# Kernel optimization log

Measured on AMD Instinct MI355X. Metric: run time of the kernel, lower is better.

The kernel has to match this reference:

```python
import jax, jax.numpy as jnp
import numpy as np

C = 512        # num_channels
HEADS = 8      # num_channels // num_head_channels
DH = 64        # num_head_channels
G = 32         # num_groups
EPS = 1e-5
SCALE = DH ** -0.25  # pre-multiplied into q and k (scale applied twice -> 1/sqrt(DH))


def setup_inputs() -> dict:
    key = jax.random.key(0)
    ks = jax.random.split(key, 10)
    B, H, W = 2, 64, 64
    def w(k):
        return jax.random.normal(k, (C, C), jnp.float32) * 0.02
    def b(k):
        return jax.random.normal(k, (C,), jnp.float32) * 0.02
    return {
        "x": jax.random.normal(ks[0], (B, C, H, W), jnp.float32),
        "gn_w": jnp.ones((C,), jnp.float32),
        "gn_b": jnp.zeros((C,), jnp.float32),
        "wq": w(ks[1]), "bq": b(ks[2]),
        "wk": w(ks[3]), "bk": b(ks[4]),
        "wv": w(ks[5]), "bv": b(ks[6]),
        "wp": w(ks[7]), "bp": b(ks[8]),
    }


def reference(x, gn_w, gn_b, wq, bq, wk, bk, wv, bv, wp, bp):
    B, Cc, H, W = x.shape
    # GroupNorm over (C/G, H, W) per group
    xr = x.reshape(B, G, Cc // G, H * W)
    mean = xr.mean(axis=(2, 3), keepdims=True)
    var = xr.var(axis=(2, 3), keepdims=True)
    h = ((xr - mean) * jax.lax.rsqrt(var + EPS)).reshape(B, Cc, H, W)
    h = h * gn_w[None, :, None, None] + gn_b[None, :, None, None]
    # B C H W -> B (H W) C
    t = h.reshape(B, Cc, H * W).transpose(0, 2, 1)
    # q/k pre-multiplied by SCALE (equivalent to pre_multiply_weights_by_scale)
    q = (t @ wq.T + bq) * SCALE
    k = (t @ wk.T + bk) * SCALE
    v = t @ wv.T + bv
    def split_heads(a):  # B HW (h d) -> B h HW d
        return a.reshape(B, H * W, HEADS, DH).transpose(0, 2, 1, 3)
    q, k, v = split_heads(q), split_heads(k), split_heads(v)
    # full HWxHW score matrix, softmax over keys
    attn = jax.nn.softmax(jnp.einsum('bhqd,bhkd->bhqk', q, k), axis=-1)
    o = jnp.einsum('bhqk,bhkd->bhqd', attn, v)
    o = o.transpose(0, 2, 1, 3).reshape(B, H * W, Cc)  # join heads
    o = o @ wp.T + bp
    # B (H W) C -> B C H W, residual
    return o.transpose(0, 2, 1).reshape(B, Cc, H, W) + x
```

## Files before the change

kernel.cpp:

```cpp
#include <hip/hip_runtime.h>

#define HWN 4096
#define CCH 512
#define NHEAD 8
#define DHD 64
#define NBATCH 2
#define QK_SCALE 0.35355339059327373f
#define LOG2E    1.4426950408889634f

using floatx4 = __attribute__((ext_vector_type(4))) float;
using bf16x8  = __attribute__((ext_vector_type(8))) short;
using bf16x4  = __attribute__((ext_vector_type(4))) short;

__device__ __forceinline__ unsigned short f2b(float f) {
  union { float f; unsigned u; } x; x.f = f;
  unsigned r = x.u + 0x7FFFu + ((x.u >> 16) & 1u);
  return (unsigned short)(r >> 16);
}

__device__ __forceinline__ float fast_exp2(float x) {
#if __has_builtin(__builtin_amdgcn_exp2f)
  return __builtin_amdgcn_exp2f(x);
#else
  return __expf(x * 0.69314718056f);
#endif
}

__device__ __forceinline__ unsigned pack_bf16_trunc(float lo, float hi) {
  return __builtin_amdgcn_perm(__float_as_uint(hi), __float_as_uint(lo), 0x07060302u);
}

__global__ __launch_bounds__(256) void gn_stats(const float* __restrict__ x,
                                                float* __restrict__ stat) {
  int bg = blockIdx.x;
  const float4* p = (const float4*)(x + (size_t)bg * 65536) + blockIdx.y * 2048;
  float s = 0.f, ss = 0.f;
  for (int i = threadIdx.x; i < 2048; i += 256) {
    float4 v = p[i];
    s  += v.x + v.y + v.z + v.w;
    ss += v.x*v.x + v.y*v.y + v.z*v.z + v.w*v.w;
  }
  for (int off = 32; off; off >>= 1) {
    s  += __shfl_xor(s, off);
    ss += __shfl_xor(ss, off);
  }
  __shared__ float red[8];
  int w = threadIdx.x >> 6;
  if ((threadIdx.x & 63) == 0) { red[w] = s; red[4 + w] = ss; }
  __syncthreads();
  if (threadIdx.x == 0) {
    float S  = red[0] + red[1] + red[2] + red[3];
    float SS = red[4] + red[5] + red[6] + red[7];
    atomicAdd(&stat[bg], S);
    atomicAdd(&stat[64 + bg], SS);
  }
}

__global__ __launch_bounds__(256) void prep_w(
    const float* __restrict__ wq, const float* __restrict__ wk,
    const float* __restrict__ wv, const float* __restrict__ wp,
    const float* __restrict__ bq, const float* __restrict__ bk,
    const float* __restrict__ bv,
    unsigned short* __restrict__ Wqkv, unsigned short* __restrict__ Wp,
    float* __restrict__ bqkv) {
  int i = blockIdx.x * 256 + threadIdx.x;
  if (i < 786432) {
    int row = i >> 9;
    float v;
    if (row < 512)       v = wq[i] * (QK_SCALE * LOG2E);
    else if (row < 1024) v = wk[i - 262144] * QK_SCALE;
    else                 v = wv[i - 524288];
    Wqkv[i] = f2b(v);
  } else if (i < 1048576) {
    Wp[i - 786432] = f2b(wp[i - 786432]);
  } else if (i < 1050112) {
    int j = i - 1048576;
    float v = (j < 512) ? bq[j] * (QK_SCALE * LOG2E)
            : (j < 1024) ? bk[j - 512] * QK_SCALE
            : bv[j - 1024];
    bqkv[j] = v;
  }
}

__global__ __launch_bounds__(256) void gn_apply(
    const float* __restrict__ x, const float* __restrict__ stat,
    const float* __restrict__ gnw, const float* __restrict__ gnb,
    unsigned short* __restrict__ t) {
  int pt = blockIdx.x & 63;
  int ct = (blockIdx.x >> 6) & 7;
  int b  = blockIdx.x >> 9;
  int c0 = ct * 64, p0 = pt * 64;
  __shared__ float tile[64][68];
  int tid = threadIdx.x;
  for (int pp = 0; pp < 4; ++pp) {
    int f = (pp * 256 + tid) * 4;
    int cl = f >> 6, pl = f & 63;
    int c = c0 + cl;
    float4 v = *(const float4*)(x + ((size_t)(b * 512 + c)) * 4096 + p0 + pl);
    int g = c >> 4;
    float S    = stat[b * 32 + g];
    float SS   = stat[64 + b * 32 + g];
    float mean = S * (1.f / 65536.f);
    float var  = SS * (1.f / 65536.f) - mean * mean;
    float rstd = rsqrtf(var + 1e-5f);
    float w  = gnw[c] * rstd;
    float bb = gnb[c] - mean * w;
    tile[cl][pl + 0] = v.x * w + bb;
    tile[cl][pl + 1] = v.y * w + bb;
    tile[cl][pl + 2] = v.z * w + bb;
    tile[cl][pl + 3] = v.w * w + bb;
  }
  __syncthreads();
  for (int pp = 0; pp < 2; ++pp) {
    int f = (pp * 256 + tid) * 8;
    int pl = f >> 6, cl = f & 63;
    unsigned short u[8];
#pragma unroll
    for (int j = 0; j < 8; ++j) u[j] = f2b(tile[cl + j][pl]);
    *(uint4*)(t + ((size_t)(b * 4096 + p0 + pl)) * 512 + c0 + cl) = *(uint4*)u;
  }
}

__global__ __launch_bounds__(256) void gemm_qkv(
    const unsigned short* __restrict__ t, const unsigned short* __restrict__ Wqkv,
    const float* __restrict__ bqkv,
    unsigned short* __restrict__ qo, unsigned short* __restrict__ ko,
    unsigned short* __restrict__ vo) {
  int M0 = blockIdx.x * 64;
  int N0 = blockIdx.y * 64;
  __shared__ unsigned short At[64][72];
  __shared__ unsigned short Bt[64][72];
  int tid = threadIdx.x, w = tid >> 6, l = tid & 63;
  int quad = l >> 4, m16 = l & 15;
  floatx4 acc[4] = {};
  for (int k0 = 0; k0 < 512; k0 += 64) {
    __syncthreads();
#pragma unroll
    for (int pp = 0; pp < 2; ++pp) {
      int f = (pp * 256 + tid) * 8;
      int r = f >> 6, c = f & 63;
      *(uint4*)&At[r][c] = *(const uint4*)(t    + (size_t)(M0 + r) * 512 + k0 + c);
      *(uint4*)&Bt[r][c] = *(const uint4*)(Wqkv + (size_t)(N0 + r) * 512 + k0 + c);
    }
    __syncthreads();
    bf16x8 af0 = *(const bf16x8*)&At[w * 16 + m16][quad * 8];
    bf16x8 af1 = *(const bf16x8*)&At[w * 16 + m16][32 + quad * 8];
#pragma unroll
    for (int nt = 0; nt < 4; ++nt) {
      bf16x8 b0 = *(const bf16x8*)&Bt[nt * 16 + m16][quad * 8];
      bf16x8 b1 = *(const bf16x8*)&Bt[nt * 16 + m16][32 + quad * 8];
      acc[nt] = __builtin_amdgcn_mfma_f32_16x16x32_bf16(af0, b0, acc[nt], 0, 0, 0);
      acc[nt] = __builtin_amdgcn_mfma_f32_16x16x32_bf16(af1, b1, acc[nt], 0, 0, 0);
    }
  }
  int which = N0 >> 9;
  int head  = (N0 & 511) >> 6;
  if (which == 2) {
    __syncthreads();
#pragma unroll
    for (int nt = 0; nt < 4; ++nt) {
      int d = nt * 16 + m16;
      float bias = bqkv[N0 + d];
#pragma unroll
      for (int r = 0; r < 4; ++r)
        At[d][w * 16 + quad * 4 + r] = f2b(acc[nt][r] + bias);
    }
    __syncthreads();
    int bb = M0 >> 12, p0 = M0 & 4095;
    unsigned short* dst = vo + ((size_t)(bb * 8 + head) * 64) * 4096;
#pragma unroll
    for (int pp = 0; pp < 2; ++pp) {
      int f = (pp * 256 + tid) * 8;
      int d = f >> 6, pl = f & 63;
      *(uint4*)(dst + (size_t)d * 4096 + p0 + pl) = *(uint4*)&At[d][pl];
    }
  } else {
    unsigned short* dst = (which == 0) ? qo : ko;
#pragma unroll
    for (int nt = 0; nt < 4; ++nt) {
      int n = N0 + nt * 16 + m16;
      float bias = bqkv[n];
      int d = n & 63;
#pragma unroll
      for (int r = 0; r < 4; ++r) {
        int m = M0 + w * 16 + quad * 4 + r;
        int b = m >> 12, p = m & 4095;
        dst[(((size_t)(b * 8 + head) * 4096 + p) << 6) + d] = f2b(acc[nt][r] + bias);
      }
    }
  }
}

__global__ __launch_bounds__(256, 4) void attn(
    const unsigned short* __restrict__ q, const unsigned short* __restrict__ k,
    const unsigned short* __restrict__ vt, unsigned short* __restrict__ o) {
  int qt = blockIdx.x;
  int bh = blockIdx.y;
  int b = bh >> 3, h = bh & 7;
  __shared__ unsigned short Kt[128][72];
  __shared__ unsigned short Vt[64][136];
  int tid = threadIdx.x, w = tid >> 6, l = tid & 63;
  int quad = l >> 4, m16 = l & 15;
  const size_t base = (size_t)bh * HWN * DHD;

  bf16x8 qf0, qf1;
  {
    int qrow = qt * 64 + w * 16 + m16;
    const unsigned short* qp = q + base + (size_t)qrow * 64 + quad * 8;
    qf0 = *(const bf16x8*)qp;
    qf1 = *(const bf16x8*)(qp + 32);
  }
  floatx4 accO[4] = {};
  float mrow = -1e30f, lrow = 0.f;

  for (int kt = 0; kt < 32; ++kt) {
    __syncthreads();
#pragma unroll
    for (int pp = 0; pp < 4; ++pp) {
      int f = (pp * 256 + tid) * 8;
      int rk = f >> 6, ck = f & 63;
      *(uint4*)&Kt[rk][ck] = *(const uint4*)(k + base + (size_t)(kt * 128 + rk) * 64 + ck);
      int rv = f >> 7, cv = f & 127;
      *(uint4*)&Vt[rv][cv] = *(const uint4*)(vt + base + (size_t)rv * 4096 + kt * 128 + cv);
    }
    __syncthreads();
    floatx4 s[8];
#pragma unroll
    for (int nt = 0; nt < 8; ++nt) {
      bf16x8 kf0 = *(const bf16x8*)&Kt[nt * 16 + m16][quad * 8];
      bf16x8 kf1 = *(const bf16x8*)&Kt[nt * 16 + m16][32 + quad * 8];
      floatx4 z = {};
      z = __builtin_amdgcn_mfma_f32_16x16x32_bf16(kf0, qf0, z, 0, 0, 0);
      s[nt] = __builtin_amdgcn_mfma_f32_16x16x32_bf16(kf1, qf1, z, 0, 0, 0);
    }
    float mx = s[0][0];
#pragma unroll
    for (int nt = 0; nt < 8; ++nt)
#pragma unroll
      for (int i = 0; i < 4; ++i) mx = fmaxf(mx, s[nt][i]);
    mx = fmaxf(mx, __shfl_xor(mx, 16));
    mx = fmaxf(mx, __shfl_xor(mx, 32));
    bool grew = mx > mrow;
    float mnew = fmaxf(mrow, mx);
    float rs = 0.f;
#pragma unroll
    for (int nt = 0; nt < 8; ++nt)
#pragma unroll
      for (int i = 0; i < 4; ++i) {
        float p = fast_exp2(s[nt][i] - mnew);
        s[nt][i] = p;
        rs += p;
      }
    rs += __shfl_xor(rs, 16);
    rs += __shfl_xor(rs, 32);
    if (__ballot(grew)) {
      float alpha = fast_exp2(mrow - mnew);
      float al0 = __shfl(alpha, quad * 4 + 0);
      float al1 = __shfl(alpha, quad * 4 + 1);
      float al2 = __shfl(alpha, quad * 4 + 2);
      float al3 = __shfl(alpha, quad * 4 + 3);
#pragma unroll
      for (int dt = 0; dt < 4; ++dt) {
        accO[dt][0] *= al0; accO[dt][1] *= al1;
        accO[dt][2] *= al2; accO[dt][3] *= al3;
      }
      lrow = lrow * alpha + rs;
    } else {
      lrow += rs;
    }
    mrow = mnew;
    bf16x4 pf[8];
#pragma unroll
    for (int nt = 0; nt < 8; ++nt) {
      union { unsigned u[2]; bf16x4 v; } pu;
      pu.u[0] = pack_bf16_trunc(s[nt][0], s[nt][1]);
      pu.u[1] = pack_bf16_trunc(s[nt][2], s[nt][3]);
      pf[nt] = pu.v;
    }
#pragma unroll
    for (int dt = 0; dt < 4; ++dt) {
#pragma unroll
      for (int nt = 0; nt < 8; ++nt) {
        bf16x4 vf = *(const bf16x4*)&Vt[dt * 16 + m16][nt * 16 + quad * 4];
        accO[dt] = __builtin_amdgcn_mfma_f32_16x16x16bf16_1k(pf[nt], vf, accO[dt], 0, 0, 0);
      }
    }
  }
  float li0 = 1.f / __shfl(lrow, quad * 4 + 0);
  float li1 = 1.f / __shfl(lrow, quad * 4 + 1);
  float li2 = 1.f / __shfl(lrow, quad * 4 + 2);
  float li3 = 1.f / __shfl(lrow, quad * 4 + 3);
#pragma unroll
  for (int dt = 0; dt < 4; ++dt) {
    int d = dt * 16 + m16;
    int qrow = qt * 64 + w * 16 + quad * 4;
    size_t rowb = ((size_t)(b * 4096 + qrow)) * 512 + h * 64 + d;
    o[rowb]           = f2b(accO[dt][0] * li0);
    o[rowb + 512]     = f2b(accO[dt][1] * li1);
    o[rowb + 1024]    = f2b(accO[dt][2] * li2);
    o[rowb + 1536]    = f2b(accO[dt][3] * li3);
  }
}

__global__ __launch_bounds__(256) void gemm_out(
    const unsigned short* __restrict__ o, const unsigned short* __restrict__ Wp,
    const float* __restrict__ bp, const float* __restrict__ x,
    float* __restrict__ out) {
  int C0 = blockIdx.x * 64, P0 = blockIdx.y * 64, b = blockIdx.z;
  __shared__ unsigned short At[64][72];
  __shared__ unsigned short Bt[64][72];
  int tid = threadIdx.x, w = tid >> 6, l = tid & 63;
  int quad = l >> 4, m16 = l & 15;
  floatx4 acc[4] = {};
  for (int k0 = 0; k0 < 512; k0 += 64) {
    __syncthreads();
#pragma unroll
    for (int pp = 0; pp < 2; ++pp) {
      int f = (pp * 256 + tid) * 8;
      int r = f >> 6, c = f & 63;
      *(uint4*)&At[r][c] = *(const uint4*)(Wp + (size_t)(C0 + r) * 512 + k0 + c);
      *(uint4*)&Bt[r][c] = *(const uint4*)(o + ((size_t)(b * 4096 + P0 + r)) * 512 + k0 + c);
    }
    __syncthreads();
    bf16x8 af0 = *(const bf16x8*)&At[w * 16 + m16][quad * 8];
    bf16x8 af1 = *(const bf16x8*)&At[w * 16 + m16][32 + quad * 8];
#pragma unroll
    for (int nt = 0; nt < 4; ++nt) {
      bf16x8 b0 = *(const bf16x8*)&Bt[nt * 16 + m16][quad * 8];
      bf16x8 b1 = *(const bf16x8*)&Bt[nt * 16 + m16][32 + quad * 8];
      acc[nt] = __builtin_amdgcn_mfma_f32_16x16x32_bf16(af0, b0, acc[nt], 0, 0, 0);
      acc[nt] = __builtin_amdgcn_mfma_f32_16x16x32_bf16(af1, b1, acc[nt], 0, 0, 0);
    }
  }
#pragma unroll
  for (int r = 0; r < 4; ++r) {
    int c = C0 + w * 16 + quad * 4 + r;
    float bias = bp[c];
#pragma unroll
    for (int nt = 0; nt < 4; ++nt) {
      int p = P0 + nt * 16 + m16;
      size_t idx = ((size_t)(b * 512 + c)) * 4096 + p;
      out[idx] = acc[nt][r] + bias + x[idx];
    }
  }
}

extern "C" void kernel_launch(void* const* d_in, const int* in_sizes, int n_in,
                              void* d_out, int out_size, void* d_ws, size_t ws_size,
                              hipStream_t stream) {
  const float* x   = (const float*)d_in[0];
  const float* gnw = (const float*)d_in[1];
  const float* gnb = (const float*)d_in[2];
  const float* wq  = (const float*)d_in[3];
  const float* bq  = (const float*)d_in[4];
  const float* wk  = (const float*)d_in[5];
  const float* bk  = (const float*)d_in[6];
  const float* wv  = (const float*)d_in[7];
  const float* bv  = (const float*)d_in[8];
  const float* wp  = (const float*)d_in[9];
  const float* bp  = (const float*)d_in[10];
  float* out = (float*)d_out;

  char* ws = (char*)d_ws;
  float* stat          = (float*)ws;          ws += 1024;
  float* bqkv          = (float*)ws;          ws += 8192;
  unsigned short* Wqkv = (unsigned short*)ws; ws += (size_t)1536 * 512 * 2;
  unsigned short* Wp   = (unsigned short*)ws; ws += (size_t)512 * 512 * 2;
  unsigned short* t    = (unsigned short*)ws; ws += (size_t)8192 * 512 * 2;
  unsigned short* qb   = (unsigned short*)ws; ws += (size_t)8192 * 512 * 2;
  unsigned short* kb   = (unsigned short*)ws; ws += (size_t)8192 * 512 * 2;
  unsigned short* vb   = (unsigned short*)ws; ws += (size_t)8192 * 512 * 2;
  unsigned short* ob   = (unsigned short*)ws; ws += (size_t)8192 * 512 * 2;

  hipMemsetAsync(stat, 0, 512, stream);
  dim3 g0(64, 8);
  gn_stats<<<g0, 256, 0, stream>>>(x, stat);
  prep_w<<<4103, 256, 0, stream>>>(wq, wk, wv, wp, bq, bk, bv, Wqkv, Wp, bqkv);
  gn_apply<<<1024, 256, 0, stream>>>(x, stat, gnw, gnb, t);
  dim3 g1(128, 24);
  gemm_qkv<<<g1, 256, 0, stream>>>(t, Wqkv, bqkv, qb, kb, vb);
  dim3 g2(64, 16);
  attn<<<g2, 256, 0, stream>>>(qb, kb, vb, ob);
  dim3 g3(8, 64, 2);
  gemm_out<<<g3, 256, 0, stream>>>(ob, Wp, bp, x, out);
}
```

Baseline: 273.0 us.

## Use 16x16x32 MFMA for PV and compute softmax row sums via MFMA

The attention kernel permutes which K rows each score MFMA covers so that the probability registers line up with the k=32 operand layout. The PV product can then use the 16x16x32 bf16 MFMA instead of twice as many 16x16x16 MFMAs. The per-row softmax denominator is now accumulated by an MFMA against a vector of ones rather than by VALU adds and cross-lane shuffles. This saves instruction count and shuffles at the cost of extra MFMA work, and the denominator is now summed from the truncated bf16 probabilities.

```diff
diff --git a/kernel.cpp b/kernel.cpp
--- a/kernel.cpp
+++ b/kernel.cpp
@@ -202,6 +202,7 @@
   int tid = threadIdx.x, w = tid >> 6, l = tid & 63;
   int quad = l >> 4, m16 = l & 15;
   const size_t base = (size_t)bh * HWN * DHD;
+  int krow_base = ((m16 >> 2) * 8) + (m16 & 3);
 
   bf16x8 qf0, qf1;
   {
@@ -210,8 +211,13 @@
     qf0 = *(const bf16x8*)qp;
     qf1 = *(const bf16x8*)(qp + 32);
   }
+  bf16x8 ones;
+#pragma unroll
+  for (int z = 0; z < 8; ++z) ones[z] = (short)0x3F80;
+
   floatx4 accO[4] = {};
-  float mrow = -1e30f, lrow = 0.f;
+  floatx4 accL = {};
+  float mrow = -1e30f;
 
   for (int kt = 0; kt < 32; ++kt) {
     __syncthreads();
@@ -226,33 +232,35 @@
     __syncthreads();
     floatx4 s[8];
 #pragma unroll
-    for (int nt = 0; nt < 8; ++nt) {
-      bf16x8 kf0 = *(const bf16x8*)&Kt[nt * 16 + m16][quad * 8];
-      bf16x8 kf1 = *(const bf16x8*)&Kt[nt * 16 + m16][32 + quad * 8];
-      floatx4 z = {};
-      z = __builtin_amdgcn_mfma_f32_16x16x32_bf16(kf0, qf0, z, 0, 0, 0);
-      s[nt] = __builtin_amdgcn_mfma_f32_16x16x32_bf16(kf1, qf1, z, 0, 0, 0);
-    }
-    float mx = s[0][0];
-#pragma unroll
-    for (int nt = 0; nt < 8; ++nt)
-#pragma unroll
-      for (int i = 0; i < 4; ++i) mx = fmaxf(mx, s[nt][i]);
+    for (int nt = 0; nt < 4; ++nt)
+#pragma unroll
+      for (int hh = 0; hh < 2; ++hh) {
+        int row = nt * 32 + hh * 4 + krow_base;
+        bf16x8 kf0 = *(const bf16x8*)&Kt[row][quad * 8];
+        bf16x8 kf1 = *(const bf16x8*)&Kt[row][32 + quad * 8];
+        floatx4 z = {};
+        z = __builtin_amdgcn_mfma_f32_16x16x32_bf16(kf0, qf0, z, 0, 0, 0);
+        s[nt * 2 + hh] = __builtin_amdgcn_mfma_f32_16x16x32_bf16(kf1, qf1, z, 0, 0, 0);
+      }
+    float m0 = fmaxf(fmaxf(s[0][0], s[0][1]), fmaxf(s[0][2], s[0][3]));
+    float m1 = fmaxf(fmaxf(s[1][0], s[1][1]), fmaxf(s[1][2], s[1][3]));
+    float m2 = fmaxf(fmaxf(s[2][0], s[2][1]), fmaxf(s[2][2], s[2][3]));
+    float m3 = fmaxf(fmaxf(s[3][0], s[3][1]), fmaxf(s[3][2], s[3][3]));
+    float m4 = fmaxf(fmaxf(s[4][0], s[4][1]), fmaxf(s[4][2], s[4][3]));
+    float m5 = fmaxf(fmaxf(s[5][0], s[5][1]), fmaxf(s[5][2], s[5][3]));
+    float m6 = fmaxf(fmaxf(s[6][0], s[6][1]), fmaxf(s[6][2], s[6][3]));
+    float m7 = fmaxf(fmaxf(s[7][0], s[7][1]), fmaxf(s[7][2], s[7][3]));
+    float mx = fmaxf(fmaxf(fmaxf(m0, m1), fmaxf(m2, m3)),
+                     fmaxf(fmaxf(m4, m5), fmaxf(m6, m7)));
     mx = fmaxf(mx, __shfl_xor(mx, 16));
     mx = fmaxf(mx, __shfl_xor(mx, 32));
     bool grew = mx > mrow;
     float mnew = fmaxf(mrow, mx);
-    float rs = 0.f;
 #pragma unroll
     for (int nt = 0; nt < 8; ++nt)
 #pragma unroll
-      for (int i = 0; i < 4; ++i) {
-        float p = fast_exp2(s[nt][i] - mnew);
-        s[nt][i] = p;
-        rs += p;
-      }
-    rs += __shfl_xor(rs, 16);
-    rs += __shfl_xor(rs, 32);
+      for (int i = 0; i < 4; ++i)
+        s[nt][i] = fast_exp2(s[nt][i] - mnew);
     if (__ballot(grew)) {
       float alpha = fast_exp2(mrow - mnew);
       float al0 = __shfl(alpha, quad * 4 + 0);
@@ -264,32 +272,35 @@
         accO[dt][0] *= al0; accO[dt][1] *= al1;
         accO[dt][2] *= al2; accO[dt][3] *= al3;
       }
-      lrow = lrow * alpha + rs;
-    } else {
-      lrow += rs;
+      accL[0] *= al0; accL[1] *= al1; accL[2] *= al2; accL[3] *= al3;
     }
     mrow = mnew;
-    bf16x4 pf[8];
-#pragma unroll
-    for (int nt = 0; nt < 8; ++nt) {
-      union { unsigned u[2]; bf16x4 v; } pu;
-      pu.u[0] = pack_bf16_trunc(s[nt][0], s[nt][1]);
-      pu.u[1] = pack_bf16_trunc(s[nt][2], s[nt][3]);
+    bf16x8 pf[4];
+#pragma unroll
+    for (int nt = 0; nt < 4; ++nt) {
+      union { unsigned u[4]; bf16x8 v; } pu;
+      pu.u[0] = pack_bf16_trunc(s[nt * 2][0],     s[nt * 2][1]);
+      pu.u[1] = pack_bf16_trunc(s[nt * 2][2],     s[nt * 2][3]);
+      pu.u[2] = pack_bf16_trunc(s[nt * 2 + 1][0], s[nt * 2 + 1][1]);
+      pu.u[3] = pack_bf16_trunc(s[nt * 2 + 1][2], s[nt * 2 + 1][3]);
       pf[nt] = pu.v;
     }
 #pragma unroll
     for (int dt = 0; dt < 4; ++dt) {
 #pragma unroll
-      for (int nt = 0; nt < 8; ++nt) {
-        bf16x4 vf = *(const bf16x4*)&Vt[dt * 16 + m16][nt * 16 + quad * 4];
-        accO[dt] = __builtin_amdgcn_mfma_f32_16x16x16bf16_1k(pf[nt], vf, accO[dt], 0, 0, 0);
+      for (int nt = 0; nt < 4; ++nt) {
+        bf16x8 vf = *(const bf16x8*)&Vt[dt * 16 + m16][nt * 32 + quad * 8];
+        accO[dt] = __builtin_amdgcn_mfma_f32_16x16x32_bf16(pf[nt], vf, accO[dt], 0, 0, 0);
       }
     }
-  }
-  float li0 = 1.f / __shfl(lrow, quad * 4 + 0);
-  float li1 = 1.f / __shfl(lrow, quad * 4 + 1);
-  float li2 = 1.f / __shfl(lrow, quad * 4 + 2);
-  float li3 = 1.f / __shfl(lrow, quad * 4 + 3);
+#pragma unroll
+    for (int nt = 0; nt < 4; ++nt)
+      accL = __builtin_amdgcn_mfma_f32_16x16x32_bf16(pf[nt], ones, accL, 0, 0, 0);
+  }
+  float li0 = 1.f / accL[0];
+  float li1 = 1.f / accL[1];
+  float li2 = 1.f / accL[2];
+  float li3 = 1.f / accL[3];
 #pragma unroll
   for (int dt = 0; dt < 4; ++dt) {
     int d = dt * 16 + m16;
```

Result: no change. 274.4 us (+0.5%).
